# Kernel tuning notes

Hardware: AMD Instinct MI355X
Metric: run time of the kernel (lower is better)

The kernel has to match this reference:

```python
import jax, jax.numpy as jnp
import numpy as np

K = 1024
D = 256
BETA = 0.25


def setup_inputs() -> dict:
    key = jax.random.key(0)
    k1, k2 = jax.random.split(key)
    inputs = jax.random.normal(k1, (16, D, 4096), dtype=jnp.float32)  # (B, D, T)
    # embedding.weight.data.uniform_(-1/K, 1/K)
    weight = jax.random.uniform(k2, (K, D), dtype=jnp.float32, minval=-1.0 / K, maxval=1.0 / K)
    return {"inputs": inputs, "weight": weight}


def reference(inputs, weight):
    B, Dd, T = inputs.shape
    x = jnp.transpose(inputs, (0, 2, 1))          # (B, T, D)
    flat = x.reshape(-1, Dd)                      # (N, D), N = B*T
    in_sqr = jnp.sum(flat * flat, axis=1, keepdims=True)     # (N, 1)
    embed_sqr = jnp.sum(weight * weight, axis=1)             # (K,)
    dis = in_sqr + embed_sqr - 2.0 * (flat @ weight.T)       # (N, K)
    ind = jnp.argmin(dis, axis=1)                            # (N,)
    quant = weight[ind].reshape(B, T, Dd)                    # gather == one-hot @ weight
    vq = jnp.mean((jax.lax.stop_gradient(quant) - x) ** 2)
    commit = jnp.mean((quant - jax.lax.stop_gradient(x)) ** 2)
    vq_loss = BETA * vq + commit
    quant_st = x + jax.lax.stop_gradient(quant - x)          # straight-through
    N = flat.shape[0]
    counts = jnp.zeros((K,), dtype=jnp.float32).at[ind].add(1.0)
    avg_probs = counts / N
    perp = jnp.exp(-jnp.sum(avg_probs * jnp.log(avg_probs + 1e-10)))
    return jnp.transpose(quant_st, (0, 2, 1)), vq_loss, perp
```

## Files before the change

### kernel.cpp

```cpp
#include <hip/hip_runtime.h>
#include <hip/hip_bf16.h>


#define DD   256
#define KK   1024
#define TT   4096
#define BBB  16
#define NROW (BBB*TT)

typedef _Float16 half8 __attribute__((ext_vector_type(8)));
typedef float f32x4 __attribute__((ext_vector_type(4)));

__device__ __forceinline__ unsigned umaxu(unsigned a, unsigned b) { return a > b ? a : b; }
__device__ __forceinline__ unsigned uminu(unsigned a, unsigned b) { return a < b ? a : b; }

__global__ void prep(const float* __restrict__ w, _Float16* __restrict__ w16,
                     unsigned* __restrict__ counts, double* __restrict__ lsum,
                     float* __restrict__ wsq) {
    int gid = blockIdx.x * 256 + threadIdx.x;
    int k = gid >> 5;
    int c = gid & 31;
    int tile = k >> 6, kc = k & 63;
    const float* src = w + (k << 8) + (c << 3);
    union { uint4 u; _Float16 h[8]; } pk;
#pragma unroll
    for (int j = 0; j < 8; ++j) pk.h[j] = (_Float16)(src[j] * 1024.0f);
    int swz = c ^ (kc & 31);
    *(uint4*)(w16 + ((size_t)tile << 14) + (kc << 8) + (swz << 3)) = pk.u;
    if (c == 0) {
        const float4* wr4 = (const float4*)(w + (k << 8));
        float s = 0.f;
#pragma unroll 8
        for (int ii = 0; ii < 64; ++ii) {
            float4 v = wr4[ii];
            s += v.x * v.x + v.y * v.y + v.z * v.z + v.w * v.w;
        }
        wsq[k] = 512.0f * s;
    }
    if (gid < KK) counts[gid] = 0u;
    if (gid == KK) *lsum = 0.0;
}

__global__ __launch_bounds__(256) void stageA(const float* __restrict__ x,
                                              const _Float16* __restrict__ w16,
                                              const float* __restrict__ wsq,
                                              uint4* __restrict__ cand) {
    __shared__ __align__(16) _Float16 wt[64 * 256];
    __shared__ __align__(16) float wsql[KK];
    int tid = threadIdx.x, bid = blockIdx.x;
    int b = bid >> 5;
    int t0 = (bid & 31) << 7;
    const float* xbase = x + ((size_t)b << 20) + t0;

    int lane = tid & 63, wv = tid >> 6;
    int n = lane & 15, q = lane >> 4;

    ((float4*)wsql)[tid] = ((const float4*)wsq)[tid];

    half8 afrag[2][8];
#pragma unroll
    for (int mt = 0; mt < 2; ++mt) {
        int rl = (wv << 5) + (mt << 4) + n;
#pragma unroll
        for (int ks = 0; ks < 8; ++ks) {
            const float* p = xbase + (((size_t)((ks << 5) + (q << 3))) << 12) + rl;
            half8 f;
#pragma unroll
            for (int j = 0; j < 8; ++j) f[j] = (_Float16)p[(size_t)j << 12];
            afrag[mt][ks] = f;
        }
    }

    unsigned b1[8], b2[8];
#pragma unroll
    for (int i = 0; i < 8; ++i) { b1[i] = 0u; b2[i] = 0u; }

    for (int wti = 0; wti < 16; ++wti) {
        __syncthreads();
        const uint4* wsrc = (const uint4*)(w16 + ((size_t)wti << 14));
#pragma unroll
        for (int it = 0; it < 8; ++it)
            ((uint4*)wt)[(it << 8) + tid] = wsrc[(it << 8) + tid];
        __syncthreads();

#pragma unroll
        for (int ct = 0; ct < 4; ++ct) {
            int kc = (ct << 4) + n;
            float csub = wsql[(wti << 6) + kc];
            half8 bfr[8];
#pragma unroll
            for (int ks = 0; ks < 8; ++ks)
                bfr[ks] = *(const half8*)(&wt[(kc << 8) + ((((ks << 2) + q) ^ (kc & 31)) << 3)]);
            f32x4 a0 = {0.f, 0.f, 0.f, 0.f};
            f32x4 a1 = {0.f, 0.f, 0.f, 0.f};
#pragma unroll
            for (int ks = 0; ks < 8; ++ks) {
                a0 = __builtin_amdgcn_mfma_f32_16x16x32_f16(afrag[0][ks], bfr[ks], a0, 0, 0, 0);
                a1 = __builtin_amdgcn_mfma_f32_16x16x32_f16(afrag[1][ks], bfr[ks], a1, 0, 0, 0);
            }
            unsigned kg = (unsigned)((wti << 6) + kc);
#pragma unroll
            for (int i = 0; i < 4; ++i) {
                float v = fmaxf(a0[i] - csub, 0.0f);
                unsigned p = (__float_as_uint(v) & 0xFFFFFC00u) | kg;
                unsigned o = b1[i];
                b2[i] = umaxu(b2[i], uminu(p, o));
                b1[i] = umaxu(o, p);
                v = fmaxf(a1[i] - csub, 0.0f);
                p = (__float_as_uint(v) & 0xFFFFFC00u) | kg;
                o = b1[4 + i];
                b2[4 + i] = umaxu(b2[4 + i], uminu(p, o));
                b1[4 + i] = umaxu(o, p);
            }
        }
    }

#pragma unroll
    for (int s = 0; s < 8; ++s) {
        unsigned v0 = b1[s], v1 = b2[s], v2 = 0u, v3 = 0u;
#pragma unroll
        for (int m = 1; m <= 8; m <<= 1) {
            unsigned e0 = __shfl_xor(v0, m);
            unsigned e1 = __shfl_xor(v1, m);
            unsigned e2 = __shfl_xor(v2, m);
            unsigned e3 = __shfl_xor(v3, m);
#pragma unroll
            for (int u = 0; u < 4; ++u) {
                unsigned e = (u == 0) ? e0 : (u == 1) ? e1 : (u == 2) ? e2 : e3;
                unsigned t;
                t = umaxu(e, v0); e = uminu(e, v0); v0 = t;
                t = umaxu(e, v1); e = uminu(e, v1); v1 = t;
                t = umaxu(e, v2); e = uminu(e, v2); v2 = t;
                v3 = umaxu(e, v3);
            }
        }
        if (n == 0) {
            int row_local = (wv << 5) + ((s >> 2) << 4) + (q << 2) + (s & 3);
            cand[(bid << 7) + row_local] = make_uint4(v0, v1, v2, v3);
        }
    }
}

#define XLS 260
__global__ __launch_bounds__(256) void stageBC(const float* __restrict__ x,
                                               const float* __restrict__ w,
                                               const uint4* __restrict__ cand,
                                               float* __restrict__ out,
                                               unsigned* __restrict__ counts,
                                               double* __restrict__ lsum) {
    __shared__ __align__(16) float xl[64 * XLS];
    __shared__ double disl[64][4];
    __shared__ int winner[64];
    __shared__ double ldis[64];
    int tid = threadIdx.x, bid = blockIdx.x;
    int b = bid >> 6, t0 = (bid & 63) << 6;
    int lane = tid & 63, wv = tid >> 6;

#pragma unroll 4
    for (int pass = 0; pass < 16; ++pass) {
        int d = (tid >> 4) + (pass << 4);
        int t4 = (tid & 15) << 2;
        float4 v = *(const float4*)(x + ((size_t)b << 20) + ((size_t)d << 12) + t0 + t4);
        xl[(t4 + 0) * XLS + d] = v.x;
        xl[(t4 + 1) * XLS + d] = v.y;
        xl[(t4 + 2) * XLS + d] = v.z;
        xl[(t4 + 3) * XLS + d] = v.w;
    }
    __syncthreads();

    int c = lane >> 4, dl = lane & 15;
    for (int rr = 0; rr < 16; ++rr) {
        int r = (wv << 4) + rr;
        int rowg = (b << 12) + t0 + r;
        unsigned ci = ((const unsigned*)cand)[((size_t)rowg << 2) + c] & 1023u;
        const float* wr = w + (ci << 8);
        double s = 0.0;
#pragma unroll
        for (int dd = 0; dd < 4; ++dd) {
            int d4 = (dd << 6) + (dl << 2);
            float4 xv = *(const float4*)(&xl[r * XLS + d4]);
            float4 wv4 = *(const float4*)(wr + d4);
            double e;
            e = (double)xv.x - (double)wv4.x; s = fma(e, e, s);
            e = (double)xv.y - (double)wv4.y; s = fma(e, e, s);
            e = (double)xv.z - (double)wv4.z; s = fma(e, e, s);
            e = (double)xv.w - (double)wv4.w; s = fma(e, e, s);
        }
#pragma unroll
        for (int m = 1; m <= 8; m <<= 1) s += __shfl_xor(s, m);
        if (dl == 0) disl[r][c] = s;
    }
    __syncthreads();

    if (tid < 64) {
        int rowg = (b << 12) + t0 + tid;
        uint4 cc = cand[rowg];
        unsigned i0 = cc.x & 1023u, i1 = cc.y & 1023u, i2 = cc.z & 1023u, i3 = cc.w & 1023u;
        double dm = disl[tid][0]; unsigned ci = i0;
        double dk;
        dk = disl[tid][1]; if (dk < dm || (dk == dm && i1 < ci)) { dm = dk; ci = i1; }
        dk = disl[tid][2]; if (dk < dm || (dk == dm && i2 < ci)) { dm = dk; ci = i2; }
        dk = disl[tid][3]; if (dk < dm || (dk == dm && i3 < ci)) { dm = dk; ci = i3; }
        winner[tid] = (int)ci;
        ldis[tid] = dm;
        atomicAdd(&counts[ci], 1u);
    }
    __syncthreads();

    float* wg = xl;
#pragma unroll 4
    for (int rp = 0; rp < 16; ++rp) {
        int r = (rp << 2) + wv;
        int win = winner[r];
        *(float4*)(&wg[r * XLS + (lane << 2)]) =
            *(const float4*)(w + (win << 8) + (lane << 2));
    }
    __syncthreads();

    {
        int t4 = (tid & 15) << 2, dr = tid >> 4;
        float* ob = out + ((size_t)b << 20) + t0 + t4;
#pragma unroll 4
        for (int pass = 0; pass < 16; ++pass) {
            int d = dr + (pass << 4);
            float4 o;
            o.x = wg[(t4 + 0) * XLS + d];
            o.y = wg[(t4 + 1) * XLS + d];
            o.z = wg[(t4 + 2) * XLS + d];
            o.w = wg[(t4 + 3) * XLS + d];
            *(float4*)(ob + ((size_t)d << 12)) = o;
        }
    }

    __syncthreads();
    if (tid < 32) ldis[tid] += ldis[tid + 32];
    __syncthreads();
    if (tid < 16) ldis[tid] += ldis[tid + 16];
    __syncthreads();
    if (tid < 8) ldis[tid] += ldis[tid + 8];
    __syncthreads();
    if (tid < 4) ldis[tid] += ldis[tid + 4];
    __syncthreads();
    if (tid < 2) ldis[tid] += ldis[tid + 2];
    __syncthreads();
    if (tid == 0) atomicAdd(lsum, ldis[0] + ldis[1]);
}

__global__ void finalize(const unsigned* __restrict__ counts,
                         const double* __restrict__ lsum,
                         float* __restrict__ out2) {
    __shared__ double part[256];
    int tid = threadIdx.x;
    double s = 0.0;
    for (int i = tid; i < KK; i += 256) {
        double p = (double)counts[i] / (double)NROW;
        s += p * log(p + 1e-10);
    }
    part[tid] = s;
    __syncthreads();
    for (int st = 128; st > 0; st >>= 1) {
        if (tid < st) part[tid] += part[tid + st];
        __syncthreads();
    }
    if (tid == 0) {
        out2[0] = (float)(1.25 * (*lsum) / ((double)NROW * (double)DD));
        out2[1] = (float)exp(-part[0]);
    }
}

extern "C" void kernel_launch(void* const* d_in, const int* in_sizes, int n_in,
                              void* d_out, int out_size, void* d_ws, size_t ws_size,
                              hipStream_t stream) {
    const float* x = (const float*)d_in[0];
    const float* w = (const float*)d_in[1];
    float* out = (float*)d_out;
    char* ws = (char*)d_ws;
    _Float16* w16    = (_Float16*)ws;
    uint4*    cnd    = (uint4*)(ws + 524288);
    unsigned* counts = (unsigned*)(ws + 1572864);
    float*    wsq    = (float*)(ws + 1576960);
    double*   lsum   = (double*)(ws + 1581056);

    prep<<<128, 256, 0, stream>>>(w, w16, counts, lsum, wsq);
    stageA<<<512, 256, 0, stream>>>(x, w16, wsq, (uint4*)cnd);
    stageBC<<<1024, 256, 0, stream>>>(x, w, (const uint4*)cnd, out, counts, lsum);
    finalize<<<1, 256, 0, stream>>>(counts, lsum, out + (size_t)NROW * DD);
}
```

Measured before the change: 208.5 us.

## Read codebook fragments directly from global memory and shrink stageBC tiles

The prep kernel now writes the fp16 codebook pre-arranged in MFMA B-fragment order. This lets stageA load each lane's fragments straight from global/L2 memory with contiguous 16-byte loads, dropping the per-tile LDS staging and its two barriers. stageBC now handles 32 rows per block instead of 64, launching twice as many blocks with less shared memory each, and the LDS row pitch changes to 257. The trade-offs are more L2 traffic in stageA, since no LDS reuse is shared across waves, and float4 LDS accesses at a 257-float pitch are no longer 16-byte aligned.

```diff
diff --git a/kernel.cpp b/kernel.cpp
--- a/kernel.cpp
+++ b/kernel.cpp
@@ -20,13 +20,14 @@
     int gid = blockIdx.x * 256 + threadIdx.x;
     int k = gid >> 5;
     int c = gid & 31;
-    int tile = k >> 6, kc = k & 63;
+    int wti = k >> 6, ct = (k >> 4) & 3, n = k & 15;
+    int ks = c >> 2, q = c & 3;
     const float* src = w + (k << 8) + (c << 3);
     union { uint4 u; _Float16 h[8]; } pk;
 #pragma unroll
     for (int j = 0; j < 8; ++j) pk.h[j] = (_Float16)(src[j] * 1024.0f);
-    int swz = c ^ (kc & 31);
-    *(uint4*)(w16 + ((size_t)tile << 14) + (kc << 8) + (swz << 3)) = pk.u;
+    size_t dst = ((((size_t)(((wti << 2) + ct) << 3) + ks) * 4 + q) * 16 + n) * 8;
+    *(uint4*)(w16 + dst) = pk.u;
     if (c == 0) {
         const float4* wr4 = (const float4*)(w + (k << 8));
         float s = 0.f;
@@ -45,7 +46,6 @@
                                               const _Float16* __restrict__ w16,
                                               const float* __restrict__ wsq,
                                               uint4* __restrict__ cand) {
-    __shared__ __align__(16) _Float16 wt[64 * 256];
     __shared__ __align__(16) float wsql[KK];
     int tid = threadIdx.x, bid = blockIdx.x;
     int b = bid >> 5;
@@ -70,27 +70,22 @@
             afrag[mt][ks] = f;
         }
     }
+    __syncthreads();
 
     unsigned b1[8], b2[8];
 #pragma unroll
     for (int i = 0; i < 8; ++i) { b1[i] = 0u; b2[i] = 0u; }
 
     for (int wti = 0; wti < 16; ++wti) {
-        __syncthreads();
-        const uint4* wsrc = (const uint4*)(w16 + ((size_t)wti << 14));
-#pragma unroll
-        for (int it = 0; it < 8; ++it)
-            ((uint4*)wt)[(it << 8) + tid] = wsrc[(it << 8) + tid];
-        __syncthreads();
-
 #pragma unroll
         for (int ct = 0; ct < 4; ++ct) {
             int kc = (ct << 4) + n;
             float csub = wsql[(wti << 6) + kc];
+            const _Float16* bbase = w16 + ((size_t)(((wti << 2) + ct) << 3) << 9) + (lane << 3);
             half8 bfr[8];
 #pragma unroll
             for (int ks = 0; ks < 8; ++ks)
-                bfr[ks] = *(const half8*)(&wt[(kc << 8) + ((((ks << 2) + q) ^ (kc & 31)) << 3)]);
+                bfr[ks] = *(const half8*)(bbase + (ks << 9));
             f32x4 a0 = {0.f, 0.f, 0.f, 0.f};
             f32x4 a1 = {0.f, 0.f, 0.f, 0.f};
 #pragma unroll
@@ -141,36 +136,41 @@
     }
 }
 
-#define XLS 260
+#define XLS 257
 __global__ __launch_bounds__(256) void stageBC(const float* __restrict__ x,
                                                const float* __restrict__ w,
                                                const uint4* __restrict__ cand,
                                                float* __restrict__ out,
                                                unsigned* __restrict__ counts,
                                                double* __restrict__ lsum) {
-    __shared__ __align__(16) float xl[64 * XLS];
-    __shared__ double disl[64][4];
-    __shared__ int winner[64];
-    __shared__ double ldis[64];
+    __shared__ __align__(16) float xl[32 * XLS];
+    __shared__ double disl[32][4];
+    __shared__ int winner[32];
+    __shared__ double ldis[32];
     int tid = threadIdx.x, bid = blockIdx.x;
-    int b = bid >> 6, t0 = (bid & 63) << 6;
+    int b = bid >> 7, t0 = (bid & 127) << 5;
     int lane = tid & 63, wv = tid >> 6;
 
-#pragma unroll 4
-    for (int pass = 0; pass < 16; ++pass) {
-        int d = (tid >> 4) + (pass << 4);
-        int t4 = (tid & 15) << 2;
-        float4 v = *(const float4*)(x + ((size_t)b << 20) + ((size_t)d << 12) + t0 + t4);
-        xl[(t4 + 0) * XLS + d] = v.x;
-        xl[(t4 + 1) * XLS + d] = v.y;
-        xl[(t4 + 2) * XLS + d] = v.z;
-        xl[(t4 + 3) * XLS + d] = v.w;
+    {
+        int dr = tid >> 3;
+        int t4 = (tid & 7) << 2;
+        const float* xb = x + ((size_t)b << 20) + t0 + t4;
+#pragma unroll
+        for (int pass = 0; pass < 8; ++pass) {
+            int d = (pass << 5) + dr;
+            float4 v = *(const float4*)(xb + ((size_t)d << 12));
+            xl[(t4 + 0) * XLS + d] = v.x;
+            xl[(t4 + 1) * XLS + d] = v.y;
+            xl[(t4 + 2) * XLS + d] = v.z;
+            xl[(t4 + 3) * XLS + d] = v.w;
+        }
     }
     __syncthreads();
 
     int c = lane >> 4, dl = lane & 15;
-    for (int rr = 0; rr < 16; ++rr) {
-        int r = (wv << 4) + rr;
+#pragma unroll
+    for (int rr = 0; rr < 8; ++rr) {
+        int r = (wv << 3) + rr;
         int rowg = (b << 12) + t0 + r;
         unsigned ci = ((const unsigned*)cand)[((size_t)rowg << 2) + c] & 1023u;
         const float* wr = w + (ci << 8);
@@ -192,7 +192,7 @@
     }
     __syncthreads();
 
-    if (tid < 64) {
+    if (tid < 32) {
         int rowg = (b << 12) + t0 + tid;
         uint4 cc = cand[rowg];
         unsigned i0 = cc.x & 1023u, i1 = cc.y & 1023u, i2 = cc.z & 1023u, i3 = cc.w & 1023u;
@@ -208,8 +208,8 @@
     __syncthreads();
 
     float* wg = xl;
-#pragma unroll 4
-    for (int rp = 0; rp < 16; ++rp) {
+#pragma unroll
+    for (int rp = 0; rp < 8; ++rp) {
         int r = (rp << 2) + wv;
         int win = winner[r];
         *(float4*)(&wg[r * XLS + (lane << 2)]) =
@@ -218,11 +218,12 @@
     __syncthreads();
 
     {
-        int t4 = (tid & 15) << 2, dr = tid >> 4;
+        int dr = tid >> 3;
+        int t4 = (tid & 7) << 2;
         float* ob = out + ((size_t)b << 20) + t0 + t4;
-#pragma unroll 4
-        for (int pass = 0; pass < 16; ++pass) {
-            int d = dr + (pass << 4);
+#pragma unroll
+        for (int pass = 0; pass < 8; ++pass) {
+            int d = (pass << 5) + dr;
             float4 o;
             o.x = wg[(t4 + 0) * XLS + d];
             o.y = wg[(t4 + 1) * XLS + d];
@@ -232,8 +233,6 @@
         }
     }
 
-    __syncthreads();
-    if (tid < 32) ldis[tid] += ldis[tid + 32];
     __syncthreads();
     if (tid < 16) ldis[tid] += ldis[tid + 16];
     __syncthreads();
@@ -283,6 +282,6 @@
 
     prep<<<128, 256, 0, stream>>>(w, w16, counts, lsum, wsq);
     stageA<<<512, 256, 0, stream>>>(x, w16, wsq, (uint4*)cnd);
-    stageBC<<<1024, 256, 0, stream>>>(x, w, (const uint4*)cnd, out, counts, lsum);
+    stageBC<<<2048, 256, 0, stream>>>(x, w, (const uint4*)cnd, out, counts, lsum);
     finalize<<<1, 256, 0, stream>>>(counts, lsum, out + (size_t)NROW * DD);
 }
```

Measured after the change: 233.1 us. 1.12x slower.
